# Performance work log

Hardware: AMD Instinct MI355X
Metric: run time of the kernel (lower is better)

## Reference

```python
import jax, jax.numpy as jnp
import numpy as np

N, D = 100000, 64        # num nodes, node feature dim
E, DE = 1600000, 64      # num edges, edge feature dim
MSG_H, MSG_OUT = 128, 64 # message MLP hidden sizes (activate_final=True)
NODE_H = 128             # node MLP hidden; final size = D (residual)
LN_EPS = 1e-5


def setup_inputs() -> dict:
    key = jax.random.key(0)
    ks = jax.random.split(key, 10)
    def glorot(k, shape):
        fan_in = shape[0]
        return jax.random.normal(k, shape, jnp.float32) / jnp.sqrt(jnp.float32(fan_in))
    return {
        "nodes": jax.random.normal(ks[0], (N, D), jnp.float32),
        "edges": jax.random.normal(ks[1], (E, DE), jnp.float32),
        "senders": jax.random.randint(ks[2], (E,), 0, N, jnp.int32),
        "receivers": jax.random.randint(ks[3], (E,), 0, N, jnp.int32),
        "msg_W1": glorot(ks[4], (2 * D + DE, MSG_H)),
        "msg_b1": jnp.zeros((MSG_H,), jnp.float32),
        "msg_W2": glorot(ks[5], (MSG_H, MSG_OUT)),
        "msg_b2": jnp.zeros((MSG_OUT,), jnp.float32),
        "node_W1": glorot(ks[6], (D + MSG_OUT, NODE_H)),
        "node_b1": jnp.zeros((NODE_H,), jnp.float32),
        "node_W2": glorot(ks[7], (NODE_H, D)),
        "node_b2": jnp.zeros((D,), jnp.float32),
        "ln_scale": jnp.ones((D,), jnp.float32),
        "ln_offset": jnp.zeros((D,), jnp.float32),
    }


def reference(nodes, edges, senders, receivers,
              msg_W1, msg_b1, msg_W2, msg_b2,
              node_W1, node_b1, node_W2, node_b2,
              ln_scale, ln_offset):
    # --- message MLP (activate_final=True) over concat(sender, receiver, edge)
    x = jnp.concatenate([nodes[senders], nodes[receivers], edges], axis=-1)  # [E, 2D+DE]
    h = jax.nn.relu(x @ msg_W1 + msg_b1)
    messages = jax.nn.relu(h @ msg_W2 + msg_b2)  # [E, MSG_OUT]
    # --- aggregate messages at receivers
    agg = jax.ops.segment_sum(messages, receivers, num_segments=nodes.shape[0])  # [N, MSG_OUT]
    # --- node update MLP (no final activation), sizes [NODE_H, D] due to residual
    y = jnp.concatenate([nodes, agg], axis=-1)  # [N, D+MSG_OUT]
    y = jax.nn.relu(y @ node_W1 + node_b1)
    y = y @ node_W2 + node_b2  # [N, D]
    # --- layer norm over last axis with scale + offset
    mean = jnp.mean(y, axis=-1, keepdims=True)
    var = jnp.var(y, axis=-1, keepdims=True)
    y = (y - mean) * jax.lax.rsqrt(var + LN_EPS) * ln_scale + ln_offset
    # --- residual connection
    return nodes + y
```

## Files before the change

### kernel.cpp

```cpp
#include <hip/hip_runtime.h>

typedef short bf16x8 __attribute__((ext_vector_type(8)));
typedef float floatx4 __attribute__((ext_vector_type(4)));
typedef unsigned short u16x4 __attribute__((ext_vector_type(4)));
typedef unsigned short u16x8 __attribute__((ext_vector_type(8)));

__device__ __forceinline__ unsigned short f2bf(float f) {
  union { float f; unsigned int u; } v;
  v.f = f;
  unsigned int u = v.u + (0x7FFFu + ((v.u >> 16) & 1u));
  return (unsigned short)(u >> 16);
}

__device__ __forceinline__ float bf2f(unsigned short h) {
  union { unsigned int u; float f; } v;
  v.u = ((unsigned int)h) << 16;
  return v.f;
}

__device__ __forceinline__ bf16x8 pack8(float4 a, float4 b) {
  u16x8 h;
  h[0] = f2bf(a.x); h[1] = f2bf(a.y); h[2] = f2bf(a.z); h[3] = f2bf(a.w);
  h[4] = f2bf(b.x); h[5] = f2bf(b.y); h[6] = f2bf(b.z); h[7] = f2bf(b.w);
  union { u16x8 u; bf16x8 s; } cv; cv.u = h; return cv.s;
}

__global__ __launch_bounds__(256) void prep_weights(
    const float* __restrict__ mW1, const float* __restrict__ mW2,
    const float* __restrict__ nW1, const float* __restrict__ nW2,
    unsigned short* __restrict__ W1f, unsigned short* __restrict__ W2f,
    unsigned short* __restrict__ NW1f, unsigned short* __restrict__ NW2f) {
  int idx = blockIdx.x * 256 + threadIdx.x;
  if (idx < 24576) {
    int j = idx & 7, n = (idx >> 3) & 127, g = idx >> 10;
    W1f[idx] = f2bf(mW1[(g * 8 + j) * 128 + n]);
  } else if (idx < 32768) {
    int t = idx - 24576;
    int j = t & 7, n = (t >> 3) & 63, g = t >> 9;
    W2f[t] = f2bf(mW2[(g * 8 + j) * 64 + n]);
  } else if (idx < 49152) {
    int t = idx - 32768;
    int j = t & 7, n = (t >> 3) & 127, g = t >> 10;
    NW1f[t] = f2bf(nW1[(g * 8 + j) * 128 + n]);
  } else if (idx < 57344) {
    int t = idx - 49152;
    int j = t & 7, n = (t >> 3) & 63, g = t >> 9;
    NW2f[t] = f2bf(nW2[(g * 8 + j) * 64 + n]);
  }
}

__global__ __launch_bounds__(256) void conv_nodes(
    const float* __restrict__ nodes, unsigned short* __restrict__ nodes_bf, int total4) {
  int i = (blockIdx.x * 256 + threadIdx.x) * 4;
  if (i < total4) {
    float4 v = *(const float4*)(nodes + i);
    u16x4 h; h[0] = f2bf(v.x); h[1] = f2bf(v.y); h[2] = f2bf(v.z); h[3] = f2bf(v.w);
    *(u16x4*)(nodes_bf + i) = h;
  }
}

__global__ __launch_bounds__(256) void hist_kernel(
    const int* __restrict__ recv, int* cnt, int E) {
  int e = blockIdx.x * 256 + threadIdx.x;
  if (e < E) atomicAdd(&cnt[recv[e]], 1);
}

__global__ __launch_bounds__(1024) void scan_blocks(
    const int* __restrict__ cnt, int* __restrict__ cur, int* __restrict__ blk, int N) {
  __shared__ int s[1024];
  int t = threadIdx.x, i = blockIdx.x * 1024 + t;
  int x = (i < N) ? cnt[i] : 0;
  s[t] = x;
  __syncthreads();
#pragma unroll
  for (int off = 1; off < 1024; off <<= 1) {
    int v = (t >= off) ? s[t - off] : 0;
    __syncthreads();
    s[t] += v;
    __syncthreads();
  }
  if (i < N) cur[i] = s[t] - x;
  if (t == 1023) blk[blockIdx.x] = s[t];
}

__global__ __launch_bounds__(128) void scan_spine(int* blk, int nb) {
  __shared__ int s[128];
  int t = threadIdx.x;
  if (nb <= 128) {
    if (t < nb) s[t] = blk[t];
    __syncthreads();
    if (t == 0) { int run = 0; for (int j = 0; j < nb; ++j) { int v = s[j]; s[j] = run; run += v; } }
    __syncthreads();
    if (t < nb) blk[t] = s[t];
  } else {
    if (t == 0) { int run = 0; for (int j = 0; j < nb; ++j) { int v = blk[j]; blk[j] = run; run += v; } }
  }
}

__global__ __launch_bounds__(1024) void scan_add(
    int* __restrict__ cur, const int* __restrict__ blk, int N) {
  int i = blockIdx.x * 1024 + threadIdx.x;
  if (i < N) cur[i] += blk[blockIdx.x];
}

__global__ __launch_bounds__(256) void scatter_kernel(
    const int* __restrict__ recv, int* cur, int* __restrict__ eid, int E) {
  int e = blockIdx.x * 256 + threadIdx.x;
  if (e < E) { int p = atomicAdd(&cur[recv[e]], 1); eid[p] = e; }
}

__global__ __launch_bounds__(256, 4) void edge_kernel_csr(
    const float* __restrict__ edges, const unsigned short* __restrict__ nodes_bf,
    const int* __restrict__ senders, const int* __restrict__ receivers,
    const int* __restrict__ eid,
    const unsigned short* __restrict__ W1f, const unsigned short* __restrict__ W2f,
    const float* __restrict__ b1, const float* __restrict__ b2,
    float* agg, int E) {
  __shared__ __align__(16) unsigned char smem[32768];
  unsigned short* Hf = (unsigned short*)smem;
  unsigned short* Ms = (unsigned short*)smem;
  int* rcvRow = (int*)(smem + 16384);

  const int tid = threadIdx.x;
  const int e0 = blockIdx.x * 128;
  const int w = tid >> 6, lane = tid & 63;
  const int col = lane & 15, quad = lane >> 4;
  const int wm = w & 1, wn = w >> 1;

  int eidv[4], sndi[4], rcvi[4];
#pragma unroll
  for (int mt = 0; mt < 4; ++mt) {
    int p = e0 + wm * 64 + mt * 16 + col;
    p = p < E ? p : E - 1;
    eidv[mt] = eid[p];
  }
#pragma unroll
  for (int mt = 0; mt < 4; ++mt) { sndi[mt] = senders[eidv[mt]]; rcvi[mt] = receivers[eidv[mt]]; }

  floatx4 z4 = {0.f, 0.f, 0.f, 0.f};
  floatx4 acc1[4][4];
#pragma unroll
  for (int mt = 0; mt < 4; ++mt)
#pragma unroll
    for (int nt = 0; nt < 4; ++nt) acc1[mt][nt] = z4;

#pragma unroll
  for (int ks = 0; ks < 4; ++ks) {
    bf16x8 a[4], b[4];
#pragma unroll
    for (int mt = 0; mt < 4; ++mt) {
      int nd = (ks < 2) ? sndi[mt] : rcvi[mt];
      a[mt] = *(const bf16x8*)&nodes_bf[(size_t)nd * 64 + (ks & 1) * 32 + quad * 8];
    }
#pragma unroll
    for (int nt = 0; nt < 4; ++nt)
      b[nt] = *(const bf16x8*)&W1f[ks * 4096 + quad * 1024 + (wn * 64 + nt * 16 + col) * 8];
#pragma unroll
    for (int mt = 0; mt < 4; ++mt)
#pragma unroll
      for (int nt = 0; nt < 4; ++nt)
        acc1[mt][nt] = __builtin_amdgcn_mfma_f32_16x16x32_bf16(a[mt], b[nt], acc1[mt][nt], 0, 0, 0);
  }
#pragma unroll
  for (int ks = 4; ks < 6; ++ks) {
    bf16x8 a[4], b[4];
#pragma unroll
    for (int mt = 0; mt < 4; ++mt) {
      const float* p = edges + (size_t)eidv[mt] * 64 + (ks - 4) * 32 + quad * 8;
      float4 v0 = *(const float4*)p;
      float4 v1 = *(const float4*)(p + 4);
      a[mt] = pack8(v0, v1);
    }
#pragma unroll
    for (int nt = 0; nt < 4; ++nt)
      b[nt] = *(const bf16x8*)&W1f[ks * 4096 + quad * 1024 + (wn * 64 + nt * 16 + col) * 8];
#pragma unroll
    for (int mt = 0; mt < 4; ++mt)
#pragma unroll
      for (int nt = 0; nt < 4; ++nt)
        acc1[mt][nt] = __builtin_amdgcn_mfma_f32_16x16x32_bf16(a[mt], b[nt], acc1[mt][nt], 0, 0, 0);
  }

#pragma unroll
  for (int nt = 0; nt < 4; ++nt) {
    float bias = b1[wn * 64 + nt * 16 + col];
    int c = wn * 64 + nt * 16 + col;
    unsigned short* dst = &Hf[((c >> 3) * 128) * 8 + (c & 7)];
#pragma unroll
    for (int mt = 0; mt < 4; ++mt)
#pragma unroll
      for (int r = 0; r < 4; ++r) {
        float v = acc1[mt][nt][r] + bias;
        v = v > 0.f ? v : 0.f;
        int row = wm * 64 + mt * 16 + quad * 4 + r;
        dst[row * 8] = f2bf(v);
      }
  }
  __syncthreads();

  floatx4 acc2[4][2];
#pragma unroll
  for (int mt = 0; mt < 4; ++mt) { acc2[mt][0] = z4; acc2[mt][1] = z4; }

#pragma unroll
  for (int ks = 0; ks < 4; ++ks) {
    bf16x8 a[4], b[2];
#pragma unroll
    for (int mt = 0; mt < 4; ++mt)
      a[mt] = *(const bf16x8*)&Hf[((ks * 4 + quad) * 128 + (wm * 64 + mt * 16 + col)) * 8];
#pragma unroll
    for (int nt = 0; nt < 2; ++nt)
      b[nt] = *(const bf16x8*)&W2f[ks * 2048 + quad * 512 + (wn * 32 + nt * 16 + col) * 8];
#pragma unroll
    for (int mt = 0; mt < 4; ++mt)
#pragma unroll
      for (int nt = 0; nt < 2; ++nt)
        acc2[mt][nt] = __builtin_amdgcn_mfma_f32_16x16x32_bf16(a[mt], b[nt], acc2[mt][nt], 0, 0, 0);
  }
  __syncthreads();

  if (tid < 128) {
    int p = e0 + tid;
    rcvRow[tid] = (p < E) ? receivers[eid[p]] : -1;
  }
  float bs0 = b2[wn * 32 + col];
  float bs1 = b2[wn * 32 + 16 + col];
#pragma unroll
  for (int mt = 0; mt < 4; ++mt)
#pragma unroll
    for (int r = 0; r < 4; ++r) {
      int row = wm * 64 + mt * 16 + quad * 4 + r;
      float v0 = acc2[mt][0][r] + bs0; v0 = v0 > 0.f ? v0 : 0.f;
      float v1 = acc2[mt][1][r] + bs1; v1 = v1 > 0.f ? v1 : 0.f;
      Ms[row * 64 + wn * 32 + col] = f2bf(v0);
      Ms[row * 64 + wn * 32 + 16 + col] = f2bf(v1);
    }
  __syncthreads();

  {
    int g = tid >> 6, c = tid & 63;
    float acc = 0.f; int prev = -1;
#pragma unroll 8
    for (int i = 0; i < 32; ++i) {
      int row = g * 32 + i;
      int rv = rcvRow[row];
      float v = bf2f(Ms[row * 64 + c]);
      if (rv != prev) {
        if (prev >= 0) atomicAdd(&agg[(size_t)prev * 64 + c], acc);
        prev = rv; acc = 0.f;
      }
      if (rv >= 0) acc += v;
    }
    if (prev >= 0) atomicAdd(&agg[(size_t)prev * 64 + c], acc);
  }
}

__global__ __launch_bounds__(256, 4) void edge_kernel(
    const float* __restrict__ edges, const unsigned short* __restrict__ nodes_bf,
    const int* __restrict__ senders, const int* __restrict__ receivers,
    const unsigned short* __restrict__ W1f, const unsigned short* __restrict__ W2f,
    const float* __restrict__ b1, const float* __restrict__ b2,
    float* agg, int E) {
  __shared__ unsigned short Hf[16 * 128 * 8];

  const int tid = threadIdx.x;
  const int e0 = blockIdx.x * 128;
  const int w = tid >> 6, lane = tid & 63;
  const int col = lane & 15, quad = lane >> 4;
  const int wm = w & 1, wn = w >> 1;

  int srow[4], sndi[4], rcvi[4];
#pragma unroll
  for (int mt = 0; mt < 4; ++mt) {
    int r = e0 + wm * 64 + mt * 16 + col;
    srow[mt] = r < E ? r : E - 1;
  }
#pragma unroll
  for (int mt = 0; mt < 4; ++mt) { sndi[mt] = senders[srow[mt]]; rcvi[mt] = receivers[srow[mt]]; }

  floatx4 z4 = {0.f, 0.f, 0.f, 0.f};
  floatx4 acc1[4][4];
#pragma unroll
  for (int mt = 0; mt < 4; ++mt)
#pragma unroll
    for (int nt = 0; nt < 4; ++nt) acc1[mt][nt] = z4;

#pragma unroll
  for (int ks = 0; ks < 4; ++ks) {
    bf16x8 a[4], b[4];
#pragma unroll
    for (int mt = 0; mt < 4; ++mt) {
      int nd = (ks < 2) ? sndi[mt] : rcvi[mt];
      a[mt] = *(const bf16x8*)&nodes_bf[(size_t)nd * 64 + (ks & 1) * 32 + quad * 8];
    }
#pragma unroll
    for (int nt = 0; nt < 4; ++nt)
      b[nt] = *(const bf16x8*)&W1f[ks * 4096 + quad * 1024 + (wn * 64 + nt * 16 + col) * 8];
#pragma unroll
    for (int mt = 0; mt < 4; ++mt)
#pragma unroll
      for (int nt = 0; nt < 4; ++nt)
        acc1[mt][nt] = __builtin_amdgcn_mfma_f32_16x16x32_bf16(a[mt], b[nt], acc1[mt][nt], 0, 0, 0);
  }
#pragma unroll
  for (int ks = 4; ks < 6; ++ks) {
    bf16x8 a[4], b[4];
#pragma unroll
    for (int mt = 0; mt < 4; ++mt) {
      const float* p = edges + (size_t)srow[mt] * 64 + (ks - 4) * 32 + quad * 8;
      float4 v0 = *(const float4*)p;
      float4 v1 = *(const float4*)(p + 4);
      a[mt] = pack8(v0, v1);
    }
#pragma unroll
    for (int nt = 0; nt < 4; ++nt)
      b[nt] = *(const bf16x8*)&W1f[ks * 4096 + quad * 1024 + (wn * 64 + nt * 16 + col) * 8];
#pragma unroll
    for (int mt = 0; mt < 4; ++mt)
#pragma unroll
      for (int nt = 0; nt < 4; ++nt)
        acc1[mt][nt] = __builtin_amdgcn_mfma_f32_16x16x32_bf16(a[mt], b[nt], acc1[mt][nt], 0, 0, 0);
  }

#pragma unroll
  for (int nt = 0; nt < 4; ++nt) {
    float bias = b1[wn * 64 + nt * 16 + col];
    int c = wn * 64 + nt * 16 + col;
    unsigned short* dst = &Hf[((c >> 3) * 128) * 8 + (c & 7)];
#pragma unroll
    for (int mt = 0; mt < 4; ++mt)
#pragma unroll
      for (int r = 0; r < 4; ++r) {
        float v = acc1[mt][nt][r] + bias;
        v = v > 0.f ? v : 0.f;
        int row = wm * 64 + mt * 16 + quad * 4 + r;
        dst[row * 8] = f2bf(v);
      }
  }
  __syncthreads();

  floatx4 acc2[4][2];
#pragma unroll
  for (int mt = 0; mt < 4; ++mt) { acc2[mt][0] = z4; acc2[mt][1] = z4; }

#pragma unroll
  for (int ks = 0; ks < 4; ++ks) {
    bf16x8 a[4], b[2];
#pragma unroll
    for (int mt = 0; mt < 4; ++mt)
      a[mt] = *(const bf16x8*)&Hf[((ks * 4 + quad) * 128 + (wm * 64 + mt * 16 + col)) * 8];
#pragma unroll
    for (int nt = 0; nt < 2; ++nt)
      b[nt] = *(const bf16x8*)&W2f[ks * 2048 + quad * 512 + (wn * 32 + nt * 16 + col) * 8];
#pragma unroll
    for (int mt = 0; mt < 4; ++mt)
#pragma unroll
      for (int nt = 0; nt < 2; ++nt)
        acc2[mt][nt] = __builtin_amdgcn_mfma_f32_16x16x32_bf16(a[mt], b[nt], acc2[mt][nt], 0, 0, 0);
  }

  float bs0 = b2[wn * 32 + col];
  float bs1 = b2[wn * 32 + 16 + col];
#pragma unroll
  for (int mt = 0; mt < 4; ++mt)
#pragma unroll
    for (int r = 0; r < 4; ++r) {
      int er = e0 + wm * 64 + mt * 16 + quad * 4 + r;
      if (er < E) {
        int rv = receivers[er];
        float v0 = acc2[mt][0][r] + bs0; v0 = v0 > 0.f ? v0 : 0.f;
        float v1 = acc2[mt][1][r] + bs1; v1 = v1 > 0.f ? v1 : 0.f;
        atomicAdd(&agg[(size_t)rv * 64 + wn * 32 + col], v0);
        atomicAdd(&agg[(size_t)rv * 64 + wn * 32 + 16 + col], v1);
      }
    }
}

__global__ __launch_bounds__(256, 4) void node_kernel(
    const float* __restrict__ nodes, const unsigned short* __restrict__ nodes_bf,
    const float* agg,
    const unsigned short* __restrict__ W1f, const unsigned short* __restrict__ W2f,
    const float* __restrict__ b1, const float* __restrict__ b2,
    const float* __restrict__ ln_s, const float* __restrict__ ln_o,
    float* out, int N) {
  __shared__ __align__(16) unsigned char smem[32768];
  unsigned short* Hf = (unsigned short*)smem;
  float (*Ls1)[2] = (float(*)[2])smem;
  float (*Ls2)[2] = (float(*)[2])(smem + 1024);

  const int tid = threadIdx.x;
  const int n0 = blockIdx.x * 128;
  const int w = tid >> 6, lane = tid & 63;
  const int col = lane & 15, quad = lane >> 4;
  const int wm = w & 1, wn = w >> 1;

  int arow[4];
#pragma unroll
  for (int mt = 0; mt < 4; ++mt) {
    int r = n0 + wm * 64 + mt * 16 + col;
    arow[mt] = r < N ? r : N - 1;
  }

  floatx4 z4 = {0.f, 0.f, 0.f, 0.f};
  floatx4 acc1[4][4];
#pragma unroll
  for (int mt = 0; mt < 4; ++mt)
#pragma unroll
    for (int nt = 0; nt < 4; ++nt) acc1[mt][nt] = z4;

#pragma unroll
  for (int ks = 0; ks < 2; ++ks) {
    bf16x8 a[4], b[4];
#pragma unroll
    for (int mt = 0; mt < 4; ++mt)
      a[mt] = *(const bf16x8*)&nodes_bf[(size_t)arow[mt] * 64 + ks * 32 + quad * 8];
#pragma unroll
    for (int nt = 0; nt < 4; ++nt)
      b[nt] = *(const bf16x8*)&W1f[ks * 4096 + quad * 1024 + (wn * 64 + nt * 16 + col) * 8];
#pragma unroll
    for (int mt = 0; mt < 4; ++mt)
#pragma unroll
      for (int nt = 0; nt < 4; ++nt)
        acc1[mt][nt] = __builtin_amdgcn_mfma_f32_16x16x32_bf16(a[mt], b[nt], acc1[mt][nt], 0, 0, 0);
  }
#pragma unroll
  for (int ks = 2; ks < 4; ++ks) {
    bf16x8 a[4], b[4];
#pragma unroll
    for (int mt = 0; mt < 4; ++mt) {
      const float* p = agg + (size_t)arow[mt] * 64 + (ks - 2) * 32 + quad * 8;
      float4 v0 = *(const float4*)p;
      float4 v1 = *(const float4*)(p + 4);
      a[mt] = pack8(v0, v1);
    }
#pragma unroll
    for (int nt = 0; nt < 4; ++nt)
      b[nt] = *(const bf16x8*)&W1f[ks * 4096 + quad * 1024 + (wn * 64 + nt * 16 + col) * 8];
#pragma unroll
    for (int mt = 0; mt < 4; ++mt)
#pragma unroll
      for (int nt = 0; nt < 4; ++nt)
        acc1[mt][nt] = __builtin_amdgcn_mfma_f32_16x16x32_bf16(a[mt], b[nt], acc1[mt][nt], 0, 0, 0);
  }

#pragma unroll
  for (int nt = 0; nt < 4; ++nt) {
    float bias = b1[wn * 64 + nt * 16 + col];
    int c = wn * 64 + nt * 16 + col;
    unsigned short* dst = &Hf[((c >> 3) * 128) * 8 + (c & 7)];
#pragma unroll
    for (int mt = 0; mt < 4; ++mt)
#pragma unroll
      for (int r = 0; r < 4; ++r) {
        float v = acc1[mt][nt][r] + bias;
        v = v > 0.f ? v : 0.f;
        int row = wm * 64 + mt * 16 + quad * 4 + r;
        dst[row * 8] = f2bf(v);
      }
  }
  __syncthreads();

  floatx4 acc2[4][2];
#pragma unroll
  for (int mt = 0; mt < 4; ++mt) { acc2[mt][0] = z4; acc2[mt][1] = z4; }

#pragma unroll
  for (int ks = 0; ks < 4; ++ks) {
    bf16x8 a[4], b[2];
#pragma unroll
    for (int mt = 0; mt < 4; ++mt)
      a[mt] = *(const bf16x8*)&Hf[((ks * 4 + quad) * 128 + (wm * 64 + mt * 16 + col)) * 8];
#pragma unroll
    for (int nt = 0; nt < 2; ++nt)
      b[nt] = *(const bf16x8*)&W2f[ks * 2048 + quad * 512 + (wn * 32 + nt * 16 + col) * 8];
#pragma unroll
    for (int mt = 0; mt < 4; ++mt)
#pragma unroll
      for (int nt = 0; nt < 2; ++nt)
        acc2[mt][nt] = __builtin_amdgcn_mfma_f32_16x16x32_bf16(a[mt], b[nt], acc2[mt][nt], 0, 0, 0);
  }
  __syncthreads();

  float y[4][2][4];
  float bs0 = b2[wn * 32 + col];
  float bs1 = b2[wn * 32 + 16 + col];
#pragma unroll
  for (int mt = 0; mt < 4; ++mt)
#pragma unroll
    for (int r = 0; r < 4; ++r) {
      y[mt][0][r] = acc2[mt][0][r] + bs0;
      y[mt][1][r] = acc2[mt][1][r] + bs1;
    }

#pragma unroll
  for (int mt = 0; mt < 4; ++mt)
#pragma unroll
    for (int r = 0; r < 4; ++r) {
      float p1 = y[mt][0][r] + y[mt][1][r];
      float p2 = y[mt][0][r] * y[mt][0][r] + y[mt][1][r] * y[mt][1][r];
#pragma unroll
      for (int m = 1; m <= 8; m <<= 1) {
        p1 += __shfl_xor(p1, m);
        p2 += __shfl_xor(p2, m);
      }
      if (col == 0) {
        int row = wm * 64 + mt * 16 + quad * 4 + r;
        Ls1[row][wn] = p1;
        Ls2[row][wn] = p2;
      }
    }
  __syncthreads();

  float lsv0 = ln_s[wn * 32 + col], lsv1 = ln_s[wn * 32 + 16 + col];
  float lov0 = ln_o[wn * 32 + col], lov1 = ln_o[wn * 32 + 16 + col];
#pragma unroll
  for (int mt = 0; mt < 4; ++mt)
#pragma unroll
    for (int r = 0; r < 4; ++r) {
      int row = wm * 64 + mt * 16 + quad * 4 + r;
      int gi = n0 + row;
      float s1 = Ls1[row][0] + Ls1[row][1];
      float s2 = Ls2[row][0] + Ls2[row][1];
      float mean = s1 * (1.f / 64.f);
      float var = s2 * (1.f / 64.f) - mean * mean;
      float rstd = rsqrtf(var + 1e-5f);
      if (gi < N) {
        int j0 = wn * 32 + col;
        float o0 = (y[mt][0][r] - mean) * rstd * lsv0 + lov0 + nodes[(size_t)gi * 64 + j0];
        float o1 = (y[mt][1][r] - mean) * rstd * lsv1 + lov1 + nodes[(size_t)gi * 64 + j0 + 16];
        out[(size_t)gi * 64 + j0] = o0;
        out[(size_t)gi * 64 + j0 + 16] = o1;
      }
    }
}

extern "C" void kernel_launch(void* const* d_in, const int* in_sizes, int n_in,
                              void* d_out, int out_size, void* d_ws, size_t ws_size,
                              hipStream_t stream) {
  const float* nodes     = (const float*)d_in[0];
  const float* edges     = (const float*)d_in[1];
  const int*   senders   = (const int*)d_in[2];
  const int*   receivers = (const int*)d_in[3];
  const float* msg_W1    = (const float*)d_in[4];
  const float* msg_b1    = (const float*)d_in[5];
  const float* msg_W2    = (const float*)d_in[6];
  const float* msg_b2    = (const float*)d_in[7];
  const float* node_W1   = (const float*)d_in[8];
  const float* node_b1   = (const float*)d_in[9];
  const float* node_W2   = (const float*)d_in[10];
  const float* node_b2   = (const float*)d_in[11];
  const float* ln_scale  = (const float*)d_in[12];
  const float* ln_offset = (const float*)d_in[13];

  const int N = in_sizes[0] / 64;
  const int E = in_sizes[2];

  unsigned short* W1f  = (unsigned short*)d_ws;
  unsigned short* W2f  = W1f + 24576;
  unsigned short* NW1f = W2f + 8192;
  unsigned short* NW2f = NW1f + 16384;
  unsigned short* nodes_bf = NW2f + 8192;

  size_t base_bytes = 114688 + (size_t)N * 128;
  int* cnt = (int*)((char*)d_ws + base_bytes);
  int* cur = cnt + N;
  int* blk = cur + N;
  int* eid = blk + 1024;
  size_t need = base_bytes + (size_t)N * 8 + 4096 + (size_t)E * 4;

  float* agg = (float*)d_out;

  hipMemsetAsync(d_out, 0, (size_t)out_size * sizeof(float), stream);
  prep_weights<<<224, 256, 0, stream>>>(msg_W1, msg_W2, node_W1, node_W2, W1f, W2f, NW1f, NW2f);
  conv_nodes<<<(N * 64 + 1023) / 1024, 256, 0, stream>>>(nodes, nodes_bf, N * 64);

  if (ws_size >= need) {
    int nb = (N + 1023) / 1024;
    hipMemsetAsync(cnt, 0, (size_t)N * sizeof(int), stream);
    hist_kernel<<<(E + 255) / 256, 256, 0, stream>>>(receivers, cnt, E);
    scan_blocks<<<nb, 1024, 0, stream>>>(cnt, cur, blk, N);
    scan_spine<<<1, 128, 0, stream>>>(blk, nb);
    scan_add<<<nb, 1024, 0, stream>>>(cur, blk, N);
    scatter_kernel<<<(E + 255) / 256, 256, 0, stream>>>(receivers, cur, eid, E);
    edge_kernel_csr<<<(E + 127) / 128, 256, 0, stream>>>(edges, nodes_bf, senders, receivers,
                                                         eid, W1f, W2f, msg_b1, msg_b2, agg, E);
  } else {
    edge_kernel<<<(E + 127) / 128, 256, 0, stream>>>(edges, nodes_bf, senders, receivers,
                                                     W1f, W2f, msg_b1, msg_b2, agg, E);
  }

  node_kernel<<<(N + 127) / 128, 256, 0, stream>>>(nodes, nodes_bf, agg, NW1f, NW2f,
                                                   node_b1, node_b2, ln_scale, ln_offset,
                                                   (float*)d_out, N);
}
```

Baseline: 1.054 ms.

## Shrink edge and node kernel tiles to 64 rows and fuse scan spine

The edge and node kernels now process 64 rows per block with all four waves splitting the output columns, instead of 128 rows on a 2x2 wave grid. This halves accumulator registers and shared memory so more blocks fit per CU (launch bounds raised to 6). The trade-off is that each block loads its weight tiles for half as many rows. The edge kernel now reuses receiver indices already held in registers rather than reloading them through eid. The separate scan spine kernel is merged into the scan-add kernel, where each block sums the preceding block totals itself, removing one launch.

```diff
diff --git a/kernel.cpp b/kernel.cpp
--- a/kernel.cpp
+++ b/kernel.cpp
@@ -83,24 +83,18 @@
   if (t == 1023) blk[blockIdx.x] = s[t];
 }
 
-__global__ __launch_bounds__(128) void scan_spine(int* blk, int nb) {
-  __shared__ int s[128];
-  int t = threadIdx.x;
-  if (nb <= 128) {
-    if (t < nb) s[t] = blk[t];
-    __syncthreads();
-    if (t == 0) { int run = 0; for (int j = 0; j < nb; ++j) { int v = s[j]; s[j] = run; run += v; } }
-    __syncthreads();
-    if (t < nb) blk[t] = s[t];
-  } else {
-    if (t == 0) { int run = 0; for (int j = 0; j < nb; ++j) { int v = blk[j]; blk[j] = run; run += v; } }
-  }
-}
-
-__global__ __launch_bounds__(1024) void scan_add(
+__global__ __launch_bounds__(1024) void scan_add_spine(
     int* __restrict__ cur, const int* __restrict__ blk, int N) {
-  int i = blockIdx.x * 1024 + threadIdx.x;
-  if (i < N) cur[i] += blk[blockIdx.x];
+  __shared__ int base;
+  int b = blockIdx.x;
+  if (threadIdx.x == 0) {
+    int run = 0;
+    for (int j = 0; j < b; ++j) run += blk[j];
+    base = run;
+  }
+  __syncthreads();
+  int i = b * 1024 + threadIdx.x;
+  if (i < N) cur[i] += base;
 }
 
 __global__ __launch_bounds__(256) void scatter_kernel(
@@ -109,61 +103,58 @@
   if (e < E) { int p = atomicAdd(&cur[recv[e]], 1); eid[p] = e; }
 }
 
-__global__ __launch_bounds__(256, 4) void edge_kernel_csr(
+__global__ __launch_bounds__(256, 6) void edge_kernel_csr(
     const float* __restrict__ edges, const unsigned short* __restrict__ nodes_bf,
     const int* __restrict__ senders, const int* __restrict__ receivers,
     const int* __restrict__ eid,
     const unsigned short* __restrict__ W1f, const unsigned short* __restrict__ W2f,
     const float* __restrict__ b1, const float* __restrict__ b2,
     float* agg, int E) {
-  __shared__ __align__(16) unsigned char smem[32768];
+  __shared__ __align__(16) unsigned char smem[16384];
   unsigned short* Hf = (unsigned short*)smem;
   unsigned short* Ms = (unsigned short*)smem;
-  int* rcvRow = (int*)(smem + 16384);
+  int* rcvRow = (int*)(smem + 8192);
 
   const int tid = threadIdx.x;
-  const int e0 = blockIdx.x * 128;
-  const int w = tid >> 6, lane = tid & 63;
+  const int e0 = blockIdx.x * 64;
+  const int wn = tid >> 6, lane = tid & 63;
   const int col = lane & 15, quad = lane >> 4;
-  const int wm = w & 1, wn = w >> 1;
-
-  int eidv[4], sndi[4], rcvi[4];
+
+  int pv[4], eidv[4], sndi[4], rcvi[4];
 #pragma unroll
   for (int mt = 0; mt < 4; ++mt) {
-    int p = e0 + wm * 64 + mt * 16 + col;
-    p = p < E ? p : E - 1;
+    pv[mt] = e0 + mt * 16 + col;
+    int p = pv[mt] < E ? pv[mt] : E - 1;
     eidv[mt] = eid[p];
   }
 #pragma unroll
   for (int mt = 0; mt < 4; ++mt) { sndi[mt] = senders[eidv[mt]]; rcvi[mt] = receivers[eidv[mt]]; }
 
   floatx4 z4 = {0.f, 0.f, 0.f, 0.f};
-  floatx4 acc1[4][4];
-#pragma unroll
-  for (int mt = 0; mt < 4; ++mt)
-#pragma unroll
-    for (int nt = 0; nt < 4; ++nt) acc1[mt][nt] = z4;
+  floatx4 acc1[4][2];
+#pragma unroll
+  for (int mt = 0; mt < 4; ++mt) { acc1[mt][0] = z4; acc1[mt][1] = z4; }
 
 #pragma unroll
   for (int ks = 0; ks < 4; ++ks) {
-    bf16x8 a[4], b[4];
+    bf16x8 a[4], b[2];
 #pragma unroll
     for (int mt = 0; mt < 4; ++mt) {
       int nd = (ks < 2) ? sndi[mt] : rcvi[mt];
       a[mt] = *(const bf16x8*)&nodes_bf[(size_t)nd * 64 + (ks & 1) * 32 + quad * 8];
     }
 #pragma unroll
-    for (int nt = 0; nt < 4; ++nt)
-      b[nt] = *(const bf16x8*)&W1f[ks * 4096 + quad * 1024 + (wn * 64 + nt * 16 + col) * 8];
-#pragma unroll
-    for (int mt = 0; mt < 4; ++mt)
-#pragma unroll
-      for (int nt = 0; nt < 4; ++nt)
+    for (int nt = 0; nt < 2; ++nt)
+      b[nt] = *(const bf16x8*)&W1f[ks * 4096 + quad * 1024 + (wn * 32 + nt * 16 + col) * 8];
+#pragma unroll
+    for (int mt = 0; mt < 4; ++mt)
+#pragma unroll
+      for (int nt = 0; nt < 2; ++nt)
         acc1[mt][nt] = __builtin_amdgcn_mfma_f32_16x16x32_bf16(a[mt], b[nt], acc1[mt][nt], 0, 0, 0);
   }
 #pragma unroll
   for (int ks = 4; ks < 6; ++ks) {
-    bf16x8 a[4], b[4];
+    bf16x8 a[4], b[2];
 #pragma unroll
     for (int mt = 0; mt < 4; ++mt) {
       const float* p = edges + (size_t)eidv[mt] * 64 + (ks - 4) * 32 + quad * 8;
@@ -172,77 +163,71 @@
       a[mt] = pack8(v0, v1);
     }
 #pragma unroll
-    for (int nt = 0; nt < 4; ++nt)
-      b[nt] = *(const bf16x8*)&W1f[ks * 4096 + quad * 1024 + (wn * 64 + nt * 16 + col) * 8];
-#pragma unroll
-    for (int mt = 0; mt < 4; ++mt)
-#pragma unroll
-      for (int nt = 0; nt < 4; ++nt)
+    for (int nt = 0; nt < 2; ++nt)
+      b[nt] = *(const bf16x8*)&W1f[ks * 4096 + quad * 1024 + (wn * 32 + nt * 16 + col) * 8];
+#pragma unroll
+    for (int mt = 0; mt < 4; ++mt)
+#pragma unroll
+      for (int nt = 0; nt < 2; ++nt)
         acc1[mt][nt] = __builtin_amdgcn_mfma_f32_16x16x32_bf16(a[mt], b[nt], acc1[mt][nt], 0, 0, 0);
   }
 
 #pragma unroll
-  for (int nt = 0; nt < 4; ++nt) {
-    float bias = b1[wn * 64 + nt * 16 + col];
-    int c = wn * 64 + nt * 16 + col;
-    unsigned short* dst = &Hf[((c >> 3) * 128) * 8 + (c & 7)];
+  for (int nt = 0; nt < 2; ++nt) {
+    int c = wn * 32 + nt * 16 + col;
+    float bias = b1[c];
+    unsigned short* dst = &Hf[((c >> 3) * 64) * 8 + (c & 7)];
 #pragma unroll
     for (int mt = 0; mt < 4; ++mt)
 #pragma unroll
       for (int r = 0; r < 4; ++r) {
         float v = acc1[mt][nt][r] + bias;
         v = v > 0.f ? v : 0.f;
-        int row = wm * 64 + mt * 16 + quad * 4 + r;
+        int row = mt * 16 + quad * 4 + r;
         dst[row * 8] = f2bf(v);
       }
   }
   __syncthreads();
 
-  floatx4 acc2[4][2];
-#pragma unroll
-  for (int mt = 0; mt < 4; ++mt) { acc2[mt][0] = z4; acc2[mt][1] = z4; }
+  floatx4 acc2[4];
+#pragma unroll
+  for (int mt = 0; mt < 4; ++mt) acc2[mt] = z4;
 
 #pragma unroll
   for (int ks = 0; ks < 4; ++ks) {
-    bf16x8 a[4], b[2];
-#pragma unroll
-    for (int mt = 0; mt < 4; ++mt)
-      a[mt] = *(const bf16x8*)&Hf[((ks * 4 + quad) * 128 + (wm * 64 + mt * 16 + col)) * 8];
-#pragma unroll
-    for (int nt = 0; nt < 2; ++nt)
-      b[nt] = *(const bf16x8*)&W2f[ks * 2048 + quad * 512 + (wn * 32 + nt * 16 + col) * 8];
-#pragma unroll
-    for (int mt = 0; mt < 4; ++mt)
-#pragma unroll
-      for (int nt = 0; nt < 2; ++nt)
-        acc2[mt][nt] = __builtin_amdgcn_mfma_f32_16x16x32_bf16(a[mt], b[nt], acc2[mt][nt], 0, 0, 0);
-  }
-  __syncthreads();
-
-  if (tid < 128) {
-    int p = e0 + tid;
-    rcvRow[tid] = (p < E) ? receivers[eid[p]] : -1;
-  }
-  float bs0 = b2[wn * 32 + col];
-  float bs1 = b2[wn * 32 + 16 + col];
+    bf16x8 a[4];
+#pragma unroll
+    for (int mt = 0; mt < 4; ++mt)
+      a[mt] = *(const bf16x8*)&Hf[((ks * 4 + quad) * 64 + mt * 16 + col) * 8];
+    bf16x8 b = *(const bf16x8*)&W2f[ks * 2048 + quad * 512 + (wn * 16 + col) * 8];
+#pragma unroll
+    for (int mt = 0; mt < 4; ++mt)
+      acc2[mt] = __builtin_amdgcn_mfma_f32_16x16x32_bf16(a[mt], b, acc2[mt], 0, 0, 0);
+  }
+  __syncthreads();
+
+  if (tid < 16) {
+#pragma unroll
+    for (int mt = 0; mt < 4; ++mt)
+      rcvRow[mt * 16 + tid] = (pv[mt] < E) ? rcvi[mt] : -1;
+  }
+  float bs = b2[wn * 16 + col];
 #pragma unroll
   for (int mt = 0; mt < 4; ++mt)
 #pragma unroll
     for (int r = 0; r < 4; ++r) {
-      int row = wm * 64 + mt * 16 + quad * 4 + r;
-      float v0 = acc2[mt][0][r] + bs0; v0 = v0 > 0.f ? v0 : 0.f;
-      float v1 = acc2[mt][1][r] + bs1; v1 = v1 > 0.f ? v1 : 0.f;
-      Ms[row * 64 + wn * 32 + col] = f2bf(v0);
-      Ms[row * 64 + wn * 32 + 16 + col] = f2bf(v1);
+      int row = mt * 16 + quad * 4 + r;
+      float v = acc2[mt][r] + bs; v = v > 0.f ? v : 0.f;
+      Ms[row * 64 + wn * 16 + col] = f2bf(v);
     }
   __syncthreads();
 
   {
-    int g = tid >> 6, c = tid & 63;
+    int c = lane;
     float acc = 0.f; int prev = -1;
-#pragma unroll 8
-    for (int i = 0; i < 32; ++i) {
-      int row = g * 32 + i;
+#pragma unroll
+    for (int i = 0; i < 16; ++i) {
+      int row = wn * 16 + i;
       int rv = rcvRow[row];
       float v = bf2f(Ms[row * 64 + c]);
       if (rv != prev) {
@@ -376,56 +361,53 @@
     }
 }
 
-__global__ __launch_bounds__(256, 4) void node_kernel(
+__global__ __launch_bounds__(256, 6) void node_kernel(
     const float* __restrict__ nodes, const unsigned short* __restrict__ nodes_bf,
     const float* agg,
     const unsigned short* __restrict__ W1f, const unsigned short* __restrict__ W2f,
     const float* __restrict__ b1, const float* __restrict__ b2,
     const float* __restrict__ ln_s, const float* __restrict__ ln_o,
     float* out, int N) {
-  __shared__ __align__(16) unsigned char smem[32768];
+  __shared__ __align__(16) unsigned char smem[16384];
   unsigned short* Hf = (unsigned short*)smem;
-  float (*Ls1)[2] = (float(*)[2])smem;
-  float (*Ls2)[2] = (float(*)[2])(smem + 1024);
+  float (*Ls1)[4] = (float(*)[4])smem;
+  float (*Ls2)[4] = (float(*)[4])(smem + 1024);
 
   const int tid = threadIdx.x;
-  const int n0 = blockIdx.x * 128;
-  const int w = tid >> 6, lane = tid & 63;
+  const int n0 = blockIdx.x * 64;
+  const int wn = tid >> 6, lane = tid & 63;
   const int col = lane & 15, quad = lane >> 4;
-  const int wm = w & 1, wn = w >> 1;
 
   int arow[4];
 #pragma unroll
   for (int mt = 0; mt < 4; ++mt) {
-    int r = n0 + wm * 64 + mt * 16 + col;
+    int r = n0 + mt * 16 + col;
     arow[mt] = r < N ? r : N - 1;
   }
 
   floatx4 z4 = {0.f, 0.f, 0.f, 0.f};
-  floatx4 acc1[4][4];
-#pragma unroll
-  for (int mt = 0; mt < 4; ++mt)
-#pragma unroll
-    for (int nt = 0; nt < 4; ++nt) acc1[mt][nt] = z4;
+  floatx4 acc1[4][2];
+#pragma unroll
+  for (int mt = 0; mt < 4; ++mt) { acc1[mt][0] = z4; acc1[mt][1] = z4; }
 
 #pragma unroll
   for (int ks = 0; ks < 2; ++ks) {
-    bf16x8 a[4], b[4];
+    bf16x8 a[4], b[2];
 #pragma unroll
     for (int mt = 0; mt < 4; ++mt)
       a[mt] = *(const bf16x8*)&nodes_bf[(size_t)arow[mt] * 64 + ks * 32 + quad * 8];
 #pragma unroll
-    for (int nt = 0; nt < 4; ++nt)
-      b[nt] = *(const bf16x8*)&W1f[ks * 4096 + quad * 1024 + (wn * 64 + nt * 16 + col) * 8];
-#pragma unroll
-    for (int mt = 0; mt < 4; ++mt)
-#pragma unroll
-      for (int nt = 0; nt < 4; ++nt)
+    for (int nt = 0; nt < 2; ++nt)
+      b[nt] = *(const bf16x8*)&W1f[ks * 4096 + quad * 1024 + (wn * 32 + nt * 16 + col) * 8];
+#pragma unroll
+    for (int mt = 0; mt < 4; ++mt)
+#pragma unroll
+      for (int nt = 0; nt < 2; ++nt)
         acc1[mt][nt] = __builtin_amdgcn_mfma_f32_16x16x32_bf16(a[mt], b[nt], acc1[mt][nt], 0, 0, 0);
   }
 #pragma unroll
   for (int ks = 2; ks < 4; ++ks) {
-    bf16x8 a[4], b[4];
+    bf16x8 a[4], b[2];
 #pragma unroll
     for (int mt = 0; mt < 4; ++mt) {
       const float* p = agg + (size_t)arow[mt] * 64 + (ks - 2) * 32 + quad * 8;
@@ -434,102 +416,92 @@
       a[mt] = pack8(v0, v1);
     }
 #pragma unroll
-    for (int nt = 0; nt < 4; ++nt)
-      b[nt] = *(const bf16x8*)&W1f[ks * 4096 + quad * 1024 + (wn * 64 + nt * 16 + col) * 8];
-#pragma unroll
-    for (int mt = 0; mt < 4; ++mt)
-#pragma unroll
-      for (int nt = 0; nt < 4; ++nt)
+    for (int nt = 0; nt < 2; ++nt)
+      b[nt] = *(const bf16x8*)&W1f[ks * 4096 + quad * 1024 + (wn * 32 + nt * 16 + col) * 8];
+#pragma unroll
+    for (int mt = 0; mt < 4; ++mt)
+#pragma unroll
+      for (int nt = 0; nt < 2; ++nt)
         acc1[mt][nt] = __builtin_amdgcn_mfma_f32_16x16x32_bf16(a[mt], b[nt], acc1[mt][nt], 0, 0, 0);
   }
 
 #pragma unroll
-  for (int nt = 0; nt < 4; ++nt) {
-    float bias = b1[wn * 64 + nt * 16 + col];
-    int c = wn * 64 + nt * 16 + col;
-    unsigned short* dst = &Hf[((c >> 3) * 128) * 8 + (c & 7)];
+  for (int nt = 0; nt < 2; ++nt) {
+    int c = wn * 32 + nt * 16 + col;
+    float bias = b1[c];
+    unsigned short* dst = &Hf[((c >> 3) * 64) * 8 + (c & 7)];
 #pragma unroll
     for (int mt = 0; mt < 4; ++mt)
 #pragma unroll
       for (int r = 0; r < 4; ++r) {
         float v = acc1[mt][nt][r] + bias;
         v = v > 0.f ? v : 0.f;
-        int row = wm * 64 + mt * 16 + quad * 4 + r;
+        int row = mt * 16 + quad * 4 + r;
         dst[row * 8] = f2bf(v);
       }
   }
   __syncthreads();
 
-  floatx4 acc2[4][2];
-#pragma unroll
-  for (int mt = 0; mt < 4; ++mt) { acc2[mt][0] = z4; acc2[mt][1] = z4; }
+  floatx4 acc2[4];
+#pragma unroll
+  for (int mt = 0; mt < 4; ++mt) acc2[mt] = z4;
 
 #pragma unroll
   for (int ks = 0; ks < 4; ++ks) {
-    bf16x8 a[4], b[2];
-#pragma unroll
-    for (int mt = 0; mt < 4; ++mt)
-      a[mt] = *(const bf16x8*)&Hf[((ks * 4 + quad) * 128 + (wm * 64 + mt * 16 + col)) * 8];
-#pragma unroll
-    for (int nt = 0; nt < 2; ++nt)
-      b[nt] = *(const bf16x8*)&W2f[ks * 2048 + quad * 512 + (wn * 32 + nt * 16 + col) * 8];
-#pragma unroll
-    for (int mt = 0; mt < 4; ++mt)
-#pragma unroll
-      for (int nt = 0; nt < 2; ++nt)
-        acc2[mt][nt] = __builtin_amdgcn_mfma_f32_16x16x32_bf16(a[mt], b[nt], acc2[mt][nt], 0, 0, 0);
-  }
-  __syncthreads();
-
-  float y[4][2][4];
-  float bs0 = b2[wn * 32 + col];
-  float bs1 = b2[wn * 32 + 16 + col];
+    bf16x8 a[4];
+#pragma unroll
+    for (int mt = 0; mt < 4; ++mt)
+      a[mt] = *(const bf16x8*)&Hf[((ks * 4 + quad) * 64 + mt * 16 + col) * 8];
+    bf16x8 b = *(const bf16x8*)&W2f[ks * 2048 + quad * 512 + (wn * 16 + col) * 8];
+#pragma unroll
+    for (int mt = 0; mt < 4; ++mt)
+      acc2[mt] = __builtin_amdgcn_mfma_f32_16x16x32_bf16(a[mt], b, acc2[mt], 0, 0, 0);
+  }
+  __syncthreads();
+
+  float y[4][4];
+  float bs = b2[wn * 16 + col];
 #pragma unroll
   for (int mt = 0; mt < 4; ++mt)
 #pragma unroll
+    for (int r = 0; r < 4; ++r) y[mt][r] = acc2[mt][r] + bs;
+
+#pragma unroll
+  for (int mt = 0; mt < 4; ++mt)
+#pragma unroll
     for (int r = 0; r < 4; ++r) {
-      y[mt][0][r] = acc2[mt][0][r] + bs0;
-      y[mt][1][r] = acc2[mt][1][r] + bs1;
-    }
-
-#pragma unroll
-  for (int mt = 0; mt < 4; ++mt)
-#pragma unroll
-    for (int r = 0; r < 4; ++r) {
-      float p1 = y[mt][0][r] + y[mt][1][r];
-      float p2 = y[mt][0][r] * y[mt][0][r] + y[mt][1][r] * y[mt][1][r];
+      float p1 = y[mt][r];
+      float p2 = y[mt][r] * y[mt][r];
 #pragma unroll
       for (int m = 1; m <= 8; m <<= 1) {
         p1 += __shfl_xor(p1, m);
         p2 += __shfl_xor(p2, m);
       }
       if (col == 0) {
-        int row = wm * 64 + mt * 16 + quad * 4 + r;
+        int row = mt * 16 + quad * 4 + r;
         Ls1[row][wn] = p1;
         Ls2[row][wn] = p2;
       }
     }
   __syncthreads();
 
-  float lsv0 = ln_s[wn * 32 + col], lsv1 = ln_s[wn * 32 + 16 + col];
-  float lov0 = ln_o[wn * 32 + col], lov1 = ln_o[wn * 32 + 16 + col];
+  float lsv = ln_s[wn * 16 + col];
+  float lov = ln_o[wn * 16 + col];
 #pragma unroll
   for (int mt = 0; mt < 4; ++mt)
 #pragma unroll
     for (int r = 0; r < 4; ++r) {
-      int row = wm * 64 + mt * 16 + quad * 4 + r;
+      int row = mt * 16 + quad * 4 + r;
       int gi = n0 + row;
-      float s1 = Ls1[row][0] + Ls1[row][1];
-      float s2 = Ls2[row][0] + Ls2[row][1];
+      float s1 = Ls1[row][0] + Ls1[row][1] + Ls1[row][2] + Ls1[row][3];
+      float s2 = Ls2[row][0] + Ls2[row][1] + Ls2[row][2] + Ls2[row][3];
       float mean = s1 * (1.f / 64.f);
       float var = s2 * (1.f / 64.f) - mean * mean;
       float rstd = rsqrtf(var + 1e-5f);
       if (gi < N) {
-        int j0 = wn * 32 + col;
-        float o0 = (y[mt][0][r] - mean) * rstd * lsv0 + lov0 + nodes[(size_t)gi * 64 + j0];
-        float o1 = (y[mt][1][r] - mean) * rstd * lsv1 + lov1 + nodes[(size_t)gi * 64 + j0 + 16];
-        out[(size_t)gi * 64 + j0] = o0;
-        out[(size_t)gi * 64 + j0 + 16] = o1;
+        int j = wn * 16 + col;
+        out[(size_t)gi * 64 + j] =
+            (y[mt][r] - mean) * rstd * lsv + lov + nodes[(size_t)gi * 64 + j];
       }
     }
 }
@@ -579,17 +551,16 @@
     hipMemsetAsync(cnt, 0, (size_t)N * sizeof(int), stream);
     hist_kernel<<<(E + 255) / 256, 256, 0, stream>>>(receivers, cnt, E);
     scan_blocks<<<nb, 1024, 0, stream>>>(cnt, cur, blk, N);
-    scan_spine<<<1, 128, 0, stream>>>(blk, nb);
-    scan_add<<<nb, 1024, 0, stream>>>(cur, blk, N);
+    scan_add_spine<<<nb, 1024, 0, stream>>>(cur, blk, N);
     scatter_kernel<<<(E + 255) / 256, 256, 0, stream>>>(receivers, cur, eid, E);
-    edge_kernel_csr<<<(E + 127) / 128, 256, 0, stream>>>(edges, nodes_bf, senders, receivers,
-                                                         eid, W1f, W2f, msg_b1, msg_b2, agg, E);
+    edge_kernel_csr<<<(E + 63) / 64, 256, 0, stream>>>(edges, nodes_bf, senders, receivers,
+                                                       eid, W1f, W2f, msg_b1, msg_b2, agg, E);
   } else {
     edge_kernel<<<(E + 127) / 128, 256, 0, stream>>>(edges, nodes_bf, senders, receivers,
                                                      W1f, W2f, msg_b1, msg_b2, agg, E);
   }
 
-  node_kernel<<<(N + 127) / 128, 256, 0, stream>>>(nodes, nodes_bf, agg, NW1f, NW2f,
-                                                   node_b1, node_b2, ln_scale, ln_offset,
-                                                   (float*)d_out, N);
-}
+  node_kernel<<<(N + 63) / 64, 256, 0, stream>>>(nodes, nodes_bf, agg, NW1f, NW2f,
+                                                 node_b1, node_b2, ln_scale, ln_offset,
+                                                 (float*)d_out, N);
+}
```

New measurement: 1.264 ms. 19.9% more time.
